# Performance work log

Hardware: AMD Instinct MI355X
Metric: run time of the kernel (lower is better)

Reference implementation:

```python
import jax, jax.numpy as jnp
import numpy as np

# ---- sRGB <-> CIELAB (D65) helpers, matching standard torch lab2rgb/rgb2lab ----
_RGB2XYZ = jnp.array([[0.412453, 0.357580, 0.180423],
                      [0.212671, 0.715160, 0.072169],
                      [0.019334, 0.119193, 0.950227]], dtype=jnp.float32)
_XYZ2RGB = jnp.array([[ 3.2404542, -1.5371385, -0.4985314],
                      [-0.9692660,  1.8760108,  0.0415560],
                      [ 0.0556434, -0.2040259,  1.0572252]], dtype=jnp.float32)
_WHITE = jnp.array([0.95047, 1.0, 1.08883], dtype=jnp.float32)
_EPS = 0.008856      # (6/29)^3
_KAPPA = 7.787

def _srgb_to_linear(c):
    safe = jnp.maximum(c, 0.04045)
    return jnp.where(c <= 0.04045, c / 12.92, ((safe + 0.055) / 1.055) ** 2.4)

def _linear_to_srgb(c):
    safe = jnp.maximum(c, 0.0031308)
    return jnp.where(c <= 0.0031308, 12.92 * c, 1.055 * safe ** (1.0 / 2.4) - 0.055)

def rgb2lab(rgb):
    lin = _srgb_to_linear(rgb)                      # [N,3]
    xyz = (lin @ _RGB2XYZ.T) / _WHITE               # [N,3]
    safe = jnp.maximum(xyz, _EPS)
    f = jnp.where(xyz > _EPS, jnp.cbrt(safe), _KAPPA * xyz + 16.0 / 116.0)
    fx, fy, fz = f[..., 0], f[..., 1], f[..., 2]
    L = 116.0 * fy - 16.0
    a = 500.0 * (fx - fy)
    b = 200.0 * (fy - fz)
    return jnp.stack([L, a, b], axis=-1)

def lab2rgb(lab):
    L, a, b = lab[..., 0], lab[..., 1], lab[..., 2]
    fy = (L + 16.0) / 116.0
    fx = fy + a / 500.0
    fz = fy - b / 200.0
    f = jnp.stack([fx, fy, fz], axis=-1)
    f3 = f ** 3
    t = jnp.where(f3 > _EPS, f3, (f - 16.0 / 116.0) / _KAPPA)
    xyz = t * _WHITE
    lin = xyz @ _XYZ2RGB.T
    return _linear_to_srgb(lin)

def _forward(x, w_seq1, b_seq1, w_seq2, b_seq2, w_lin, b_lin,
             w_comb, b_comb, w_logd, b_logd, w_final, b_final):
    # lab branch
    seq = jnp.tanh(x @ w_seq1 + b_seq1) @ w_seq2 + b_seq2        # [N,3]
    lin = x @ w_lin + b_lin                                      # [N,3]
    final_lab = jnp.concatenate([lin, seq], axis=-1) @ w_comb + b_comb
    # log-density branch
    x_rgb = lab2rgb(x)
    log_density = -jnp.log10(x_rgb)
    model_processed = log_density @ w_logd + b_logd
    back_to_lab = rgb2lab(10.0 ** model_processed)
    return jnp.concatenate([final_lab, back_to_lab], axis=-1) @ w_final + b_final


def setup_inputs() -> dict:
    key = jax.random.key(0)
    ks = jax.random.split(key, 13)
    N, H = 2_097_152, 64

    def lin_init(kw, kb, fan_in, fan_out):
        bound = 1.0 / np.sqrt(fan_in)
        w = jax.random.uniform(kw, (fan_in, fan_out), minval=-bound, maxval=bound, dtype=jnp.float32)
        b = jax.random.uniform(kb, (fan_out,), minval=-bound, maxval=bound, dtype=jnp.float32)
        return w, b

    # valid Lab inputs: sample sRGB away from 0/1 then convert
    rgb = jax.random.uniform(ks[0], (N, 3), minval=0.05, maxval=0.95, dtype=jnp.float32)
    x = rgb2lab(rgb)

    kk = jax.random.split(ks[1], 12)
    w_seq1, b_seq1 = lin_init(kk[0], kk[1], 3, H)
    w_seq2, b_seq2 = lin_init(kk[2], kk[3], H, 3)
    w_lin, b_lin = lin_init(kk[4], kk[5], 3, 3)
    w_comb, b_comb = lin_init(kk[6], kk[7], 6, 3)
    w_logd, b_logd = lin_init(kk[8], kk[9], 3, 3)
    w_final, b_final = lin_init(kk[10], kk[11], 6, 3)
    return {"x": x,
            "w_seq1": w_seq1, "b_seq1": b_seq1, "w_seq2": w_seq2, "b_seq2": b_seq2,
            "w_lin": w_lin, "b_lin": b_lin, "w_comb": w_comb, "b_comb": b_comb,
            "w_logd": w_logd, "b_logd": b_logd, "w_final": w_final, "b_final": b_final}


def reference(x, w_seq1, b_seq1, w_seq2, b_seq2, w_lin, b_lin,
              w_comb, b_comb, w_logd, b_logd, w_final, b_final):
    return _forward(x, w_seq1, b_seq1, w_seq2, b_seq2, w_lin, b_lin,
                    w_comb, b_comb, w_logd, b_logd, w_final, b_final)
```

## Files before the change

kernel.cpp:

```cpp
#include <hip/hip_runtime.h>

__device__ __forceinline__ float fexp2(float x) { return __builtin_amdgcn_exp2f(x); }
__device__ __forceinline__ float flog2(float x) { return __builtin_amdgcn_logf(x); }
__device__ __forceinline__ float ffma (float a, float b, float c) { return __builtin_fmaf(a, b, c); }

#define LAB_EPS 0.008856f
#define F16_116 0.13793103448275862f
#define TSCALE  11.3137085f
#define TCLAMP  45.2547f

__global__ __launch_bounds__(256) void fused_kernel(
    const float* __restrict__ x,
    const float* __restrict__ w_seq1, const float* __restrict__ b_seq1,
    const float* __restrict__ w_seq2, const float* __restrict__ b_seq2,
    const float* __restrict__ w_lin,  const float* __restrict__ b_lin,
    const float* __restrict__ w_comb, const float* __restrict__ b_comb,
    const float* __restrict__ w_logd, const float* __restrict__ b_logd,
    const float* __restrict__ w_final,const float* __restrict__ b_final,
    float* __restrict__ out, int n)
{
    __shared__ float  gtab[2048];
    __shared__ float4 wlds[128];
    __shared__ float  smlds[33];

    const int tid = threadIdx.x;

    for (int k = tid; k < 2048; k += 256) {
        const float su = sqrtf((k + 0.5f) * (1.0f / 128.0f));
        gtab[k] = tanhf(su) / (su * TSCALE);
    }

    if (tid < 64) {
        const int j = tid;
        float H3[9];
        for (int i = 0; i < 3; ++i)
            for (int c = 0; c < 3; ++c) {
                float h = 0.f;
                for (int m = 0; m < 3; ++m) h += w_comb[(i + 3) * 3 + m] * w_final[m * 3 + c];
                H3[i * 3 + c] = h;
            }
        const float w0 = w_seq2[j * 3 + 0], w1 = w_seq2[j * 3 + 1], w2 = w_seq2[j * 3 + 2];
        wlds[2 * j]     = make_float4(w_seq1[j] * TSCALE, w_seq1[64 + j] * TSCALE,
                                      w_seq1[128 + j] * TSCALE, b_seq1[j] * TSCALE);
        wlds[2 * j + 1] = make_float4(w0 * H3[0] + w1 * H3[3] + w2 * H3[6],
                                      w0 * H3[1] + w1 * H3[4] + w2 * H3[7],
                                      w0 * H3[2] + w1 * H3[5] + w2 * H3[8], 0.f);
        if (j == 0) {
            float G[9], Wfb[9];
            for (int i = 0; i < 3; ++i)
                for (int c = 0; c < 3; ++c) {
                    float gg = 0.f;
                    for (int m = 0; m < 3; ++m) gg += w_comb[i * 3 + m] * w_final[m * 3 + c];
                    G[i * 3 + c] = gg;
                }
            for (int k = 0; k < 3; ++k)
                for (int c = 0; c < 3; ++c) {
                    float s = 0.f;
                    for (int i = 0; i < 3; ++i) s += w_lin[k * 3 + i] * G[i * 3 + c];
                    smlds[k * 3 + c] = s;
                    Wfb[k * 3 + c]   = w_final[(k + 3) * 3 + c];
                    smlds[18 + k * 3 + c] = w_logd[k * 3 + c];
                }
            for (int c = 0; c < 3; ++c) {
                smlds[9 + c]     = 500.0f * Wfb[3 + c];
                smlds[9 + 3 + c] = 116.0f * Wfb[c] - 500.0f * Wfb[3 + c] + 200.0f * Wfb[6 + c];
                smlds[9 + 6 + c] = -200.0f * Wfb[6 + c];
                float s = b_final[c] - 16.0f * Wfb[c];
                for (int i = 0; i < 3; ++i)
                    s += b_lin[i] * G[i * 3 + c] + b_seq2[i] * H3[i * 3 + c]
                       + b_comb[i] * w_final[i * 3 + c];
                smlds[27 + c] = b_logd[c];
                smlds[30 + c] = s;
            }
        }
    }
    __syncthreads();

    const int g = blockIdx.x * blockDim.x + tid;
    if (g * 4 >= n) return;

    const float4* xin = reinterpret_cast<const float4*>(x) + (size_t)g * 3;
    const float4 v0 = xin[0], v1 = xin[1], v2 = xin[2];
    const float xs[4][3] = {{v0.x, v0.y, v0.z}, {v0.w, v1.x, v1.y},
                            {v1.z, v1.w, v2.x}, {v2.y, v2.z, v2.w}};

    float acc[4][3];
#pragma unroll
    for (int p = 0; p < 4; ++p) { acc[p][0] = 0.f; acc[p][1] = 0.f; acc[p][2] = 0.f; }

#pragma unroll 4
    for (int j = 0; j < 64; ++j) {
        const float4 wa = wlds[2 * j];
        const float4 wb = wlds[2 * j + 1];
#pragma unroll
        for (int p = 0; p < 4; ++p) {
            float t = ffma(xs[p][0], wa.x, ffma(xs[p][1], wa.y, ffma(xs[p][2], wa.z, wa.w)));
            t = fminf(fmaxf(t, -TCLAMP), TCLAMP);
            const float u = t * t;
            const int idx = (int)u;
            const float h = t * gtab[idx];
            acc[p][0] = ffma(h, wb.x, acc[p][0]);
            acc[p][1] = ffma(h, wb.y, acc[p][1]);
            acc[p][2] = ffma(h, wb.z, acc[p][2]);
        }
    }

    float A[9], U[9], Wld[9], bld[3], cv[3];
#pragma unroll
    for (int i = 0; i < 9; ++i) { A[i] = smlds[i]; U[i] = smlds[9 + i]; Wld[i] = smlds[18 + i]; }
#pragma unroll
    for (int i = 0; i < 3; ++i) { bld[i] = smlds[27 + i]; cv[i] = smlds[30 + i]; }

    float ov[12];
#pragma unroll
    for (int p = 0; p < 4; ++p) {
        const float L = xs[p][0], aa = xs[p][1], bb = xs[p][2];
        const float fy = (L + 16.0f) * (1.0f / 116.0f);
        const float fx = ffma(aa,  0.002f, fy);
        const float fz = ffma(bb, -0.005f, fy);
        float rgb[3];
        {
            const float f3x = fx * fx * fx, f3y = fy * fy * fy, f3z = fz * fz * fz;
            const float tx = f3x > LAB_EPS ? f3x : (fx - F16_116) * (1.0f / 7.787f);
            const float ty = f3y > LAB_EPS ? f3y : (fy - F16_116) * (1.0f / 7.787f);
            const float tz = f3z > LAB_EPS ? f3z : (fz - F16_116) * (1.0f / 7.787f);
            const float X = tx * 0.95047f, Y = ty, Z = tz * 1.08883f;
            const float linv[3] = {
                 3.2404542f * X - 1.5371385f * Y - 0.4985314f * Z,
                -0.9692660f * X + 1.8760108f * Y + 0.0415560f * Z,
                 0.0556434f * X - 0.2040259f * Y + 1.0572252f * Z};
#pragma unroll
            for (int c = 0; c < 3; ++c) {
                const float cc = linv[c];
                const float lo = 12.92f * cc;
                const float hi = ffma(1.055f,
                                      fexp2(flog2(fmaxf(cc, 0.0031308f)) * (1.0f / 2.4f)),
                                      -0.055f);
                rgb[c] = cc <= 0.0031308f ? lo : hi;
            }
        }
        const float ld0 = -0.30102999566398120f * flog2(rgb[0]);
        const float ld1 = -0.30102999566398120f * flog2(rgb[1]);
        const float ld2 = -0.30102999566398120f * flog2(rgb[2]);
        float lin2[3];
#pragma unroll
        for (int c = 0; c < 3; ++c) {
            const float mp  = ffma(ld0, Wld[c], ffma(ld1, Wld[3 + c], ffma(ld2, Wld[6 + c], bld[c])));
            const float r10 = fexp2(mp * 3.3219280948873623f);
            const float lo  = r10 * (1.0f / 12.92f);
            const float base = (fmaxf(r10, 0.04045f) + 0.055f) * (1.0f / 1.055f);
            const float hi  = fexp2(2.4f * flog2(base));
            lin2[c] = r10 <= 0.04045f ? lo : hi;
        }
        const float X2 = (0.412453f * lin2[0] + 0.357580f * lin2[1] + 0.180423f * lin2[2]) * (1.0f / 0.95047f);
        const float Y2 =  0.212671f * lin2[0] + 0.715160f * lin2[1] + 0.072169f * lin2[2];
        const float Z2 = (0.019334f * lin2[0] + 0.119193f * lin2[1] + 0.950227f * lin2[2]) * (1.0f / 1.08883f);
        const float fX = X2 > LAB_EPS ? fexp2(flog2(fmaxf(X2, LAB_EPS)) * (1.0f / 3.0f)) : ffma(7.787f, X2, F16_116);
        const float fY = Y2 > LAB_EPS ? fexp2(flog2(fmaxf(Y2, LAB_EPS)) * (1.0f / 3.0f)) : ffma(7.787f, Y2, F16_116);
        const float fZ = Z2 > LAB_EPS ? fexp2(flog2(fmaxf(Z2, LAB_EPS)) * (1.0f / 3.0f)) : ffma(7.787f, Z2, F16_116);
#pragma unroll
        for (int c = 0; c < 3; ++c) {
            float o = cv[c];
            o = ffma(L,  A[c],     o);
            o = ffma(aa, A[3 + c], o);
            o = ffma(bb, A[6 + c], o);
            o += acc[p][c];
            o = ffma(fX, U[c],     o);
            o = ffma(fY, U[3 + c], o);
            o = ffma(fZ, U[6 + c], o);
            ov[p * 3 + c] = o;
        }
    }

    float4* op = reinterpret_cast<float4*>(out) + (size_t)g * 3;
#pragma unroll
    for (int i = 0; i < 3; ++i)
        op[i] = make_float4(ov[4 * i], ov[4 * i + 1], ov[4 * i + 2], ov[4 * i + 3]);
}

extern "C" void kernel_launch(void* const* d_in, const int* in_sizes, int n_in,
                              void* d_out, int out_size, void* d_ws, size_t ws_size,
                              hipStream_t stream)
{
    const float* x       = (const float*)d_in[0];
    const float* w_seq1  = (const float*)d_in[1];
    const float* b_seq1  = (const float*)d_in[2];
    const float* w_seq2  = (const float*)d_in[3];
    const float* b_seq2  = (const float*)d_in[4];
    const float* w_lin   = (const float*)d_in[5];
    const float* b_lin   = (const float*)d_in[6];
    const float* w_comb  = (const float*)d_in[7];
    const float* b_comb  = (const float*)d_in[8];
    const float* w_logd  = (const float*)d_in[9];
    const float* b_logd  = (const float*)d_in[10];
    const float* w_final = (const float*)d_in[11];
    const float* b_final = (const float*)d_in[12];
    float* outp = (float*)d_out;

    const int n = in_sizes[0] / 3;
    const int threads = 256;
    const int total_threads = (n + 3) / 4;
    const int blocks = (total_threads + threads - 1) / threads;

    fused_kernel<<<blocks, threads, 0, stream>>>(
        x, w_seq1, b_seq1, w_seq2, b_seq2, w_lin, b_lin, w_comb, b_comb,
        w_logd, b_logd, w_final, b_final, outp, n);
}
```

Before: 141.1 us.

## Replace LDS tanh table with exp2/rcp tanh using packed FMA, two points per thread

Drops the shared-memory tanh lookup table and evaluates tanh as 1 - 2/(exp2(k*t)+1), folding the scale into the first-layer weights. The hidden-layer math is vectorised with packed two-wide FMAs, and each thread now handles 2 points instead of 4, with float2 loads and stores. This removes the table build and the LDS gathers, but adds two transcendental ops per hidden unit and launches twice as many threads.

Result: no change. 140.7 us (-0.3%).

```diff
diff --git a/kernel.cpp b/kernel.cpp
--- a/kernel.cpp
+++ b/kernel.cpp
@@ -1,13 +1,17 @@
 #include <hip/hip_runtime.h>
+
+typedef float v2f __attribute__((ext_vector_type(2)));
 
 __device__ __forceinline__ float fexp2(float x) { return __builtin_amdgcn_exp2f(x); }
 __device__ __forceinline__ float flog2(float x) { return __builtin_amdgcn_logf(x); }
+__device__ __forceinline__ float frcp (float x) { return __builtin_amdgcn_rcpf(x); }
 __device__ __forceinline__ float ffma (float a, float b, float c) { return __builtin_fmaf(a, b, c); }
+__device__ __forceinline__ v2f  splat(float s) { v2f v; v.x = s; v.y = s; return v; }
+__device__ __forceinline__ v2f  pkfma(v2f a, v2f b, v2f c) { return __builtin_elementwise_fma(a, b, c); }
 
 #define LAB_EPS 0.008856f
 #define F16_116 0.13793103448275862f
-#define TSCALE  11.3137085f
-#define TCLAMP  45.2547f
+#define TANH_K  2.8853900817779268f
 
 __global__ __launch_bounds__(256) void fused_kernel(
     const float* __restrict__ x,
@@ -19,17 +23,10 @@
     const float* __restrict__ w_final,const float* __restrict__ b_final,
     float* __restrict__ out, int n)
 {
-    __shared__ float  gtab[2048];
     __shared__ float4 wlds[128];
     __shared__ float  smlds[33];
 
     const int tid = threadIdx.x;
-
-    for (int k = tid; k < 2048; k += 256) {
-        const float su = sqrtf((k + 0.5f) * (1.0f / 128.0f));
-        gtab[k] = tanhf(su) / (su * TSCALE);
-    }
-
     if (tid < 64) {
         const int j = tid;
         float H3[9];
@@ -40,8 +37,8 @@
                 H3[i * 3 + c] = h;
             }
         const float w0 = w_seq2[j * 3 + 0], w1 = w_seq2[j * 3 + 1], w2 = w_seq2[j * 3 + 2];
-        wlds[2 * j]     = make_float4(w_seq1[j] * TSCALE, w_seq1[64 + j] * TSCALE,
-                                      w_seq1[128 + j] * TSCALE, b_seq1[j] * TSCALE);
+        wlds[2 * j]     = make_float4(w_seq1[j] * TANH_K, w_seq1[64 + j] * TANH_K,
+                                      w_seq1[128 + j] * TANH_K, b_seq1[j] * TANH_K);
         wlds[2 * j + 1] = make_float4(w0 * H3[0] + w1 * H3[3] + w2 * H3[6],
                                       w0 * H3[1] + w1 * H3[4] + w2 * H3[7],
                                       w0 * H3[2] + w1 * H3[5] + w2 * H3[8], 0.f);
@@ -77,32 +74,33 @@
     __syncthreads();
 
     const int g = blockIdx.x * blockDim.x + tid;
-    if (g * 4 >= n) return;
-
-    const float4* xin = reinterpret_cast<const float4*>(x) + (size_t)g * 3;
-    const float4 v0 = xin[0], v1 = xin[1], v2 = xin[2];
-    const float xs[4][3] = {{v0.x, v0.y, v0.z}, {v0.w, v1.x, v1.y},
-                            {v1.z, v1.w, v2.x}, {v2.y, v2.z, v2.w}};
-
-    float acc[4][3];
-#pragma unroll
-    for (int p = 0; p < 4; ++p) { acc[p][0] = 0.f; acc[p][1] = 0.f; acc[p][2] = 0.f; }
+    if (g * 2 >= n) return;
+
+    const float2* xin = reinterpret_cast<const float2*>(x) + (size_t)g * 3;
+    const float2 v0 = xin[0], v1 = xin[1], v2 = xin[2];
+    v2f xs2[3];
+    xs2[0].x = v0.x; xs2[0].y = v1.y;
+    xs2[1].x = v0.y; xs2[1].y = v2.x;
+    xs2[2].x = v1.x; xs2[2].y = v2.y;
+
+    v2f acc2[3];
+#pragma unroll
+    for (int c = 0; c < 3; ++c) acc2[c] = splat(0.f);
 
 #pragma unroll 4
     for (int j = 0; j < 64; ++j) {
         const float4 wa = wlds[2 * j];
         const float4 wb = wlds[2 * j + 1];
-#pragma unroll
-        for (int p = 0; p < 4; ++p) {
-            float t = ffma(xs[p][0], wa.x, ffma(xs[p][1], wa.y, ffma(xs[p][2], wa.z, wa.w)));
-            t = fminf(fmaxf(t, -TCLAMP), TCLAMP);
-            const float u = t * t;
-            const int idx = (int)u;
-            const float h = t * gtab[idx];
-            acc[p][0] = ffma(h, wb.x, acc[p][0]);
-            acc[p][1] = ffma(h, wb.y, acc[p][1]);
-            acc[p][2] = ffma(h, wb.z, acc[p][2]);
-        }
+        v2f t = pkfma(xs2[0], splat(wa.x),
+                pkfma(xs2[1], splat(wa.y),
+                pkfma(xs2[2], splat(wa.z), splat(wa.w))));
+        v2f e; e.x = fexp2(t.x); e.y = fexp2(t.y);
+        v2f ep = e + splat(1.0f);
+        v2f r; r.x = frcp(ep.x); r.y = frcp(ep.y);
+        v2f h = pkfma(splat(-2.0f), r, splat(1.0f));
+        acc2[0] = pkfma(h, splat(wb.x), acc2[0]);
+        acc2[1] = pkfma(h, splat(wb.y), acc2[1]);
+        acc2[2] = pkfma(h, splat(wb.z), acc2[2]);
     }
 
     float A[9], U[9], Wld[9], bld[3], cv[3];
@@ -111,10 +109,15 @@
 #pragma unroll
     for (int i = 0; i < 3; ++i) { bld[i] = smlds[27 + i]; cv[i] = smlds[30 + i]; }
 
-    float ov[12];
-#pragma unroll
-    for (int p = 0; p < 4; ++p) {
-        const float L = xs[p][0], aa = xs[p][1], bb = xs[p][2];
+    float ov[6];
+#pragma unroll
+    for (int p = 0; p < 2; ++p) {
+        const float L  = p ? xs2[0].y : xs2[0].x;
+        const float aa = p ? xs2[1].y : xs2[1].x;
+        const float bb = p ? xs2[2].y : xs2[2].x;
+        const float a0 = p ? acc2[0].y : acc2[0].x;
+        const float a1 = p ? acc2[1].y : acc2[1].x;
+        const float a2 = p ? acc2[2].y : acc2[2].x;
         const float fy = (L + 16.0f) * (1.0f / 116.0f);
         const float fx = ffma(aa,  0.002f, fy);
         const float fz = ffma(bb, -0.005f, fy);
@@ -164,7 +167,7 @@
             o = ffma(L,  A[c],     o);
             o = ffma(aa, A[3 + c], o);
             o = ffma(bb, A[6 + c], o);
-            o += acc[p][c];
+            o += (c == 0 ? a0 : (c == 1 ? a1 : a2));
             o = ffma(fX, U[c],     o);
             o = ffma(fY, U[3 + c], o);
             o = ffma(fZ, U[6 + c], o);
@@ -172,10 +175,10 @@
         }
     }
 
-    float4* op = reinterpret_cast<float4*>(out) + (size_t)g * 3;
-#pragma unroll
-    for (int i = 0; i < 3; ++i)
-        op[i] = make_float4(ov[4 * i], ov[4 * i + 1], ov[4 * i + 2], ov[4 * i + 3]);
+    float2* op = reinterpret_cast<float2*>(out) + (size_t)g * 3;
+    op[0] = make_float2(ov[0], ov[1]);
+    op[1] = make_float2(ov[2], ov[3]);
+    op[2] = make_float2(ov[4], ov[5]);
 }
 
 extern "C" void kernel_launch(void* const* d_in, const int* in_sizes, int n_in,
@@ -199,7 +202,7 @@
 
     const int n = in_sizes[0] / 3;
     const int threads = 256;
-    const int total_threads = (n + 3) / 4;
+    const int total_threads = (n + 1) / 2;
     const int blocks = (total_threads + threads - 1) / threads;
 
     fused_kernel<<<blocks, threads, 0, stream>>>(
```
